# Performance work log

Measured on AMD Instinct MI355X. Metric: run time of the kernel, lower is better.

Reference implementation:

```python
import jax, jax.numpy as jnp
import numpy as np

N_HEADS = 16
D_HEAD = 64
TOKENS_PER_FRAME = 128
ROPE_THETA = 10000.0


def setup_inputs() -> dict:
    key = jax.random.key(0)
    ks = jax.random.split(key, 4)
    B, L, D = 2, 2048, 1024
    x = jax.random.normal(ks[0], (B, L, D), dtype=jnp.float32)
    W_qkv = jax.random.normal(ks[1], (3 * D, D), dtype=jnp.float32) * (1.0 / np.sqrt(D))
    b_qkv = jnp.zeros((3 * D,), dtype=jnp.float32)
    W_out = jax.random.normal(ks[2], (D, D), dtype=jnp.float32) * (1.0 / np.sqrt(D))
    b_out = jnp.zeros((D,), dtype=jnp.float32)
    q_gamma = jnp.ones((D_HEAD,), dtype=jnp.float32)
    k_gamma = jnp.ones((D_HEAD,), dtype=jnp.float32)
    return {"x": x, "W_qkv": W_qkv, "b_qkv": b_qkv, "W_out": W_out,
            "b_out": b_out, "q_gamma": q_gamma, "k_gamma": k_gamma}


def _rms_norm(t, gamma, eps=1e-6):
    # RMSNorm over the head dim (QKNorm)
    var = jnp.mean(jnp.square(t), axis=-1, keepdims=True)
    return t * jax.lax.rsqrt(var + eps) * gamma


def _rope(t, pos):
    # t: [B,H,L,dh], pos: [L] absolute positions (with kv-cache offset applied)
    dh = t.shape[-1]
    half = dh // 2
    inv_freq = 1.0 / (ROPE_THETA ** (jnp.arange(half, dtype=jnp.float32) / half))
    angles = pos[:, None].astype(jnp.float32) * inv_freq[None, :]  # [L, half]
    cos = jnp.cos(angles)[None, None]  # [1,1,L,half]
    sin = jnp.sin(angles)[None, None]
    t1, t2 = t[..., :half], t[..., half:]
    return jnp.concatenate([t1 * cos - t2 * sin, t2 * cos + t1 * sin], axis=-1)


def _block_causal_mask(L, tokens_per_frame, n_cached=0):
    total = n_cached + L
    n_frames = total // tokens_per_frame
    fq = (jnp.arange(L) + n_cached) // tokens_per_frame          # [L] query frames
    fk = jnp.arange(total) // tokens_per_frame                    # [total] key frames
    allow = fk[None, :] <= fq[:, None]
    allow &= ~((fq[:, None] == n_frames - 1) & (fk[None, :] == 0))
    return allow  # [L, total] bool


def reference(x, W_qkv, b_qkv, W_out, b_out, q_gamma, k_gamma):
    B, L, D = x.shape
    H, dh = N_HEADS, D_HEAD
    qkv = x @ W_qkv.T + b_qkv                                    # [B,L,3D]
    qkv = qkv.reshape(B, L, 3, H, dh).transpose(2, 0, 3, 1, 4)   # [3,B,H,L,dh]
    q, k, v = qkv[0], qkv[1], qkv[2]
    q = _rms_norm(q, q_gamma)
    k = _rms_norm(k, k_gamma)
    offset = 0  # no kv_cache (prefill)
    pos = jnp.arange(L) + offset
    q = _rope(q, pos)
    k = _rope(k, jnp.arange(offset + L))
    scale = 1.0 / np.sqrt(dh)
    scores = jnp.einsum('bhqd,bhkd->bhqk', q, k) * scale
    mask = _block_causal_mask(L, TOKENS_PER_FRAME, offset)        # [L, L+offset]
    scores = jnp.where(mask[None, None], scores, jnp.finfo(scores.dtype).min)
    probs = jax.nn.softmax(scores, axis=-1)
    attn = jnp.einsum('bhqk,bhkd->bhqd', probs, v)                # [B,H,L,dh]
    attn = attn.transpose(0, 2, 1, 3).reshape(B, L, D)
    return attn @ W_out.T + b_out
```

## Files before the change

kernel.cpp:

```cpp
#include <hip/hip_runtime.h>
#include <hip/hip_bf16.h>

typedef __bf16 bf16x8 __attribute__((ext_vector_type(8)));
typedef __bf16 bf16x4 __attribute__((ext_vector_type(4)));
typedef float  f32x4  __attribute__((ext_vector_type(4)));

#define GLOBAL_AS __attribute__((address_space(1)))
#define LDS_AS    __attribute__((address_space(3)))

__device__ __forceinline__ void glds16(const void* g, void* l) {
  __builtin_amdgcn_global_load_lds((const GLOBAL_AS void*)g, (LDS_AS void*)l, 16, 0, 0);
}

__global__ __launch_bounds__(256) void prep_kernel(
    const float* __restrict__ a, __bf16* __restrict__ da, int na4,
    const float* __restrict__ b, __bf16* __restrict__ db, int nb4,
    const float* __restrict__ c, __bf16* __restrict__ dc, int nc4,
    float2* __restrict__ tab) {
  int i = blockIdx.x * 256 + threadIdx.x;
  const float* s; __bf16* d; int j = i;
  if (i < na4) { s = a; d = da; }
  else if ((j = i - na4) < nb4) { s = b; d = db; }
  else if ((j = i - na4 - nb4) < nc4) { s = c; d = dc; }
  else {
    j = i - na4 - nb4 - nc4;
    if (j < 65536) {
      int l = j >> 5, jj = j & 31;
      float inv = 1.0f / powf(10000.0f, (float)jj * (1.0f / 32.0f));
      float ang = (float)l * inv;
      tab[j] = make_float2(cosf(ang), sinf(ang));
    }
    return;
  }
  float4 f = ((const float4*)s)[j];
  bf16x4 o;
  o[0] = (__bf16)f.x; o[1] = (__bf16)f.y; o[2] = (__bf16)f.z; o[3] = (__bf16)f.w;
  ((bf16x4*)d)[j] = o;
}

template <int EPI>
__global__ __launch_bounds__(256) void gemm_bt(
    const __bf16* __restrict__ A, const __bf16* __restrict__ Bm, int K, int nbn,
    const float* __restrict__ bias,
    __bf16* __restrict__ qo, __bf16* __restrict__ ko, __bf16* __restrict__ vo,
    float* __restrict__ out,
    const float* __restrict__ qg, const float* __restrict__ kg,
    const float2* __restrict__ tab) {
  __shared__ __bf16 As[128 * 32];
  __shared__ __bf16 Bs[128 * 32];
  const int t = threadIdx.x;
  const int nwg = gridDim.x;
  const int id = blockIdx.x;
  const int swz = (id & 7) * (nwg >> 3) + (id >> 3);
  const int bn = swz % nbn, bm = swz / nbn;
  const int lane = t & 63, w = t >> 6;
  const int wr = w >> 1, wc = w & 1;
  const int lr = lane & 15, lg = lane >> 4;
  const size_t rowA0 = (size_t)bm * 128, rowB0 = (size_t)bn * 128;

  f32x4 acc[4][4] = {};

  for (int k0 = 0; k0 < K; k0 += 32) {
    __syncthreads();
#pragma unroll
    for (int i = 0; i < 2; ++i) {
      int c = t + i * 256;
      int rr = c >> 2, c8 = (c & 3) * 8;
      glds16(A + (rowA0 + rr) * K + k0 + c8, As + c * 8);
      glds16(Bm + (rowB0 + rr) * K + k0 + c8, Bs + c * 8);
    }
    __syncthreads();
    bf16x8 af[4], bfr[4];
#pragma unroll
    for (int i = 0; i < 4; ++i) {
      af[i]  = *(const bf16x8*)&As[(wr * 64 + i * 16 + lr) * 32 + lg * 8];
      bfr[i] = *(const bf16x8*)&Bs[(wc * 64 + i * 16 + lr) * 32 + lg * 8];
    }
#pragma unroll
    for (int mi = 0; mi < 4; ++mi)
#pragma unroll
      for (int ni = 0; ni < 4; ++ni)
        acc[mi][ni] = __builtin_amdgcn_mfma_f32_16x16x32_bf16(af[mi], bfr[ni], acc[mi][ni], 0, 0, 0);
  }

  if constexpr (EPI == 0) {
    const int sect = bn >> 3;
    const int h = (bn * 2 + wc) & 15;
    float bbv[4];
#pragma unroll
    for (int ni = 0; ni < 4; ++ni) bbv[ni] = bias[bn * 128 + wc * 64 + ni * 16 + lr];
    if (sect < 2) {
      __bf16* dst = sect ? ko : qo;
      const float* g = sect ? kg : qg;
      float gam[4];
#pragma unroll
      for (int ni = 0; ni < 4; ++ni) gam[ni] = g[ni * 16 + lr];
#pragma unroll
      for (int mi = 0; mi < 4; ++mi) {
#pragma unroll
        for (int r = 0; r < 4; ++r) {
          int m = bm * 128 + wr * 64 + mi * 16 + lg * 4 + r;
          int b_ = m >> 11, l = m & 2047;
          float v0 = acc[mi][0][r] + bbv[0];
          float v1 = acc[mi][1][r] + bbv[1];
          float v2 = acc[mi][2][r] + bbv[2];
          float v3 = acc[mi][3][r] + bbv[3];
          float ss = v0 * v0 + v1 * v1 + v2 * v2 + v3 * v3;
          ss += __shfl_xor(ss, 1);
          ss += __shfl_xor(ss, 2);
          ss += __shfl_xor(ss, 4);
          ss += __shfl_xor(ss, 8);
          float rinv = rsqrtf(ss * (1.0f / 64.0f) + 1e-6f);
          v0 *= rinv * gam[0]; v1 *= rinv * gam[1];
          v2 *= rinv * gam[2]; v3 *= rinv * gam[3];
          float2 cs0 = tab[l * 32 + lr];
          float2 cs1 = tab[l * 32 + 16 + lr];
          float o0 = v0 * cs0.x - v2 * cs0.y;
          float o2 = v2 * cs0.x + v0 * cs0.y;
          float o1 = v1 * cs1.x - v3 * cs1.y;
          float o3 = v3 * cs1.x + v1 * cs1.y;
          size_t base = ((size_t)(b_ * 16 + h) * 2048 + l) * 64;
          dst[base + lr]      = (__bf16)o0;
          dst[base + 16 + lr] = (__bf16)o1;
          dst[base + 32 + lr] = (__bf16)o2;
          dst[base + 48 + lr] = (__bf16)o3;
        }
      }
    } else {
#pragma unroll
      for (int mi = 0; mi < 4; ++mi) {
#pragma unroll
        for (int ni = 0; ni < 4; ++ni) {
          int d = ni * 16 + lr;
#pragma unroll
          for (int r = 0; r < 4; ++r) {
            int m = bm * 128 + wr * 64 + mi * 16 + lg * 4 + r;
            int b_ = m >> 11, l = m & 2047;
            vo[((size_t)((b_ * 16 + h) * 64 + d)) * 2048 + l] = (__bf16)(acc[mi][ni][r] + bbv[ni]);
          }
        }
      }
    }
  } else {
#pragma unroll
    for (int mi = 0; mi < 4; ++mi) {
      int m0 = bm * 128 + wr * 64 + mi * 16 + lg * 4;
#pragma unroll
      for (int ni = 0; ni < 4; ++ni) {
        int n = bn * 128 + wc * 64 + ni * 16 + lr;
        float bb = bias[n];
#pragma unroll
        for (int r = 0; r < 4; ++r)
          out[(size_t)(m0 + r) * 1024 + n] = acc[mi][ni][r] + bb;
      }
    }
  }
}

__global__ __launch_bounds__(256) void attn_kernel(
    const __bf16* __restrict__ qb, const __bf16* __restrict__ kb,
    const __bf16* __restrict__ vT, __bf16* __restrict__ ob) {
  __shared__ char smem[49152];
  char* Qs = smem;
  char* Ps = smem;

  const int id = blockIdx.x;
  const int rank = (id < 256) ? id : 767 - id;
  const int fq = rank >> 5;
  const int bh = rank & 31;
  const int t = threadIdx.x;
  const int lane = t & 63;
  const int w = t >> 6;
  const int lr = lane & 15, lg = lane >> 4;
  const size_t hoff = (size_t)bh * (2048 * 64);

  const int fkStart = (fq == 15) ? 2 : 0;
  const int fkEnd = (fq + 1) * 2;

#pragma unroll
  for (int i = 0; i < 4; ++i) {
    int c = t + i * 256;
    int row = c >> 3, sl = c & 7;
    int sp = sl ^ (row & 7);
    glds16(qb + hoff + (size_t)(fq * 128 + row) * 64 + sp * 8, Qs + c * 16);
  }
  {
    char* Kd = smem + 16384;
    char* Vd = smem + 32768;
#pragma unroll
    for (int i = 0; i < 2; ++i) {
      int c = t + i * 256;
      int row = c >> 3, sl = c & 7;
      int sp = sl ^ (row & 7);
      glds16(kb + hoff + (size_t)(fkStart * 64 + row) * 64 + sp * 8, Kd + c * 16);
      glds16(vT + hoff + (size_t)row * 2048 + fkStart * 64 + sp * 8, Vd + c * 16);
    }
  }
  bf16x8 kr[2], vr[2];
  if (fkStart + 1 < fkEnd) {
#pragma unroll
    for (int i = 0; i < 2; ++i) {
      int c = t + i * 256;
      int row = c >> 3, sl = c & 7;
      int sp = sl ^ (row & 7);
      kr[i] = *(const bf16x8*)(kb + hoff + (size_t)((fkStart + 1) * 64 + row) * 64 + sp * 8);
      vr[i] = *(const bf16x8*)(vT + hoff + (size_t)row * 2048 + (fkStart + 1) * 64 + sp * 8);
    }
  }
  __syncthreads();

  bf16x8 aq[2][2];
#pragma unroll
  for (int kk = 0; kk < 2; ++kk)
#pragma unroll
    for (int mf = 0; mf < 2; ++mf) {
      int row = w * 32 + mf * 16 + lr;
      aq[kk][mf] = *(const bf16x8*)(Qs + row * 128 + (((kk * 4 + lg) ^ (row & 7)) << 4));
    }
  __syncthreads();

  f32x4 acc[2][4] = {};
  float m_run[2] = {-INFINITY, -INFINITY};
  float l_run[2] = {0.0f, 0.0f};

  int cur = 0;
  for (int fk = fkStart; fk < fkEnd; ++fk) {
    char* Kc = smem + 16384 + cur * 8192;
    char* Vc = smem + 32768 + cur * 8192;
    if (fk + 1 < fkEnd) {
      char* Kd = smem + 16384 + (cur ^ 1) * 8192;
      char* Vd = smem + 32768 + (cur ^ 1) * 8192;
#pragma unroll
      for (int i = 0; i < 2; ++i) {
        int c = t + i * 256;
        *(bf16x8*)(Kd + c * 16) = kr[i];
        *(bf16x8*)(Vd + c * 16) = vr[i];
      }
    }
    if (fk + 2 < fkEnd) {
#pragma unroll
      for (int i = 0; i < 2; ++i) {
        int c = t + i * 256;
        int row = c >> 3, sl = c & 7;
        int sp = sl ^ (row & 7);
        kr[i] = *(const bf16x8*)(kb + hoff + (size_t)((fk + 2) * 64 + row) * 64 + sp * 8);
        vr[i] = *(const bf16x8*)(vT + hoff + (size_t)row * 2048 + (fk + 2) * 64 + sp * 8);
      }
    }

    f32x4 st[2][4] = {};
    __builtin_amdgcn_s_setprio(1);
#pragma unroll
    for (int kk = 0; kk < 2; ++kk) {
#pragma unroll
      for (int nf = 0; nf < 4; ++nf) {
        int rk = nf * 16 + lr;
        bf16x8 bk = *(const bf16x8*)(Kc + rk * 128 + (((kk * 4 + lg) ^ (rk & 7)) << 4));
        st[0][nf] = __builtin_amdgcn_mfma_f32_16x16x32_bf16(bk, aq[kk][0], st[0][nf], 0, 0, 0);
        st[1][nf] = __builtin_amdgcn_mfma_f32_16x16x32_bf16(bk, aq[kk][1], st[1][nf], 0, 0, 0);
      }
    }
    __builtin_amdgcn_s_setprio(0);

#pragma unroll
    for (int mf = 0; mf < 2; ++mf) {
      float mx = st[mf][0][0];
#pragma unroll
      for (int nf = 0; nf < 4; ++nf)
#pragma unroll
        for (int r = 0; r < 4; ++r) mx = fmaxf(mx, st[mf][nf][r]);
      mx *= 0.125f;
      mx = fmaxf(mx, __shfl_xor(mx, 16));
      mx = fmaxf(mx, __shfl_xor(mx, 32));
      float mnew = m_run[mf], cr = 1.0f;
      if (__any(mx > m_run[mf] + 8.0f)) {
        mnew = fmaxf(m_run[mf], mx);
        cr = __expf(m_run[mf] - mnew);
#pragma unroll
        for (int df = 0; df < 4; ++df) acc[mf][df] *= cr;
      }
      float lsum = 0.0f;
#pragma unroll
      for (int nf = 0; nf < 4; ++nf)
#pragma unroll
        for (int r = 0; r < 4; ++r) {
          float p = __expf(st[mf][nf][r] * 0.125f - mnew);
          st[mf][nf][r] = p;
          lsum += p;
        }
      lsum += __shfl_xor(lsum, 16);
      lsum += __shfl_xor(lsum, 32);
      l_run[mf] = l_run[mf] * cr + lsum;
      m_run[mf] = mnew;

#pragma unroll
      for (int nf = 0; nf < 4; ++nf) {
        int row = w * 32 + mf * 16 + lr;
        bf16x4 pw;
#pragma unroll
        for (int r = 0; r < 4; ++r) pw[r] = (__bf16)st[mf][nf][r];
        int slot = nf * 2 + (lg >> 1);
        *(bf16x4*)(Ps + row * 128 + (((slot ^ (row & 7)) << 4) | ((lg & 1) * 8))) = pw;
      }
    }

    __builtin_amdgcn_s_setprio(1);
#pragma unroll
    for (int kk = 0; kk < 2; ++kk) {
      bf16x8 ap[2];
#pragma unroll
      for (int mf = 0; mf < 2; ++mf) {
        int row = w * 32 + mf * 16 + lr;
        ap[mf] = *(const bf16x8*)(Ps + row * 128 + (((kk * 4 + lg) ^ (row & 7)) << 4));
      }
#pragma unroll
      for (int df = 0; df < 4; ++df) {
        int rv = df * 16 + lr;
        bf16x8 av = *(const bf16x8*)(Vc + rv * 128 + (((kk * 4 + lg) ^ (rv & 7)) << 4));
        acc[0][df] = __builtin_amdgcn_mfma_f32_16x16x32_bf16(av, ap[0], acc[0][df], 0, 0, 0);
        acc[1][df] = __builtin_amdgcn_mfma_f32_16x16x32_bf16(av, ap[1], acc[1][df], 0, 0, 0);
      }
    }
    __builtin_amdgcn_s_setprio(0);

    __syncthreads();
    cur ^= 1;
  }

  const int b = bh >> 4, h = bh & 15;
#pragma unroll
  for (int mf = 0; mf < 2; ++mf) {
    float rl = 1.0f / l_run[mf];
    int l = fq * 128 + w * 32 + mf * 16 + lr;
#pragma unroll
    for (int df = 0; df < 4; ++df) {
      bf16x4 ov;
#pragma unroll
      for (int r = 0; r < 4; ++r) ov[r] = (__bf16)(acc[mf][df][r] * rl);
      int d0 = df * 16 + lg * 4;
      *(bf16x4*)(ob + ((size_t)(b * 2048 + l)) * 1024 + h * 64 + d0) = ov;
    }
  }
}

extern "C" void kernel_launch(void* const* d_in, const int* in_sizes, int n_in,
                              void* d_out, int out_size, void* d_ws, size_t ws_size,
                              hipStream_t stream) {
  (void)in_sizes; (void)n_in; (void)out_size; (void)ws_size;
  const float* x    = (const float*)d_in[0];
  const float* Wqkv = (const float*)d_in[1];
  const float* bqkv = (const float*)d_in[2];
  const float* Wout = (const float*)d_in[3];
  const float* bout = (const float*)d_in[4];
  const float* qg   = (const float*)d_in[5];
  const float* kg   = (const float*)d_in[6];

  char* ws = (char*)d_ws;
  __bf16* xb   = (__bf16*)(ws);
  __bf16* wqb  = (__bf16*)(ws + 8388608);
  __bf16* wob  = (__bf16*)(ws + 14680064);
  __bf16* qbuf = (__bf16*)(ws + 16777216);
  __bf16* kbuf = (__bf16*)(ws + 25165824);
  __bf16* vbuf = (__bf16*)(ws + 33554432);
  __bf16* aob  = (__bf16*)(ws + 41943040);
  float2* rtab = (float2*)(ws + 50331648);

  prep_kernel<<<8448, 256, 0, stream>>>(x, xb, 1048576, Wqkv, wqb, 786432,
                                        Wout, wob, 262144, rtab);
  gemm_bt<0><<<768, 256, 0, stream>>>(xb, wqb, 1024, 24, bqkv, qbuf, kbuf, vbuf, nullptr,
                                      qg, kg, rtab);
  attn_kernel<<<512, 256, 0, stream>>>(qbuf, kbuf, vbuf, aob);
  gemm_bt<1><<<256, 256, 0, stream>>>(aob, wob, 1024, 8, bout, nullptr, nullptr, nullptr,
                                      (float*)d_out, nullptr, nullptr, nullptr);
}
```

Before: 203.7 us.

## Split attention into single-wave blocks loading K/V directly from global memory

```diff
diff --git a/kernel.cpp b/kernel.cpp
--- a/kernel.cpp
+++ b/kernel.cpp
@@ -95,24 +95,37 @@
       float gam[4];
 #pragma unroll
       for (int ni = 0; ni < 4; ++ni) gam[ni] = g[ni * 16 + lr];
+      float ss[4][4];
+#pragma unroll
+      for (int mi = 0; mi < 4; ++mi)
+#pragma unroll
+        for (int r = 0; r < 4; ++r) {
+          float s = 0.0f;
+#pragma unroll
+          for (int ni = 0; ni < 4; ++ni) {
+            acc[mi][ni][r] += bbv[ni];
+            s += acc[mi][ni][r] * acc[mi][ni][r];
+          }
+          ss[mi][r] = s;
+        }
+#pragma unroll
+      for (int step = 1; step <= 8; step <<= 1)
+#pragma unroll
+        for (int mi = 0; mi < 4; ++mi)
+#pragma unroll
+          for (int r = 0; r < 4; ++r)
+            ss[mi][r] += __shfl_xor(ss[mi][r], step);
 #pragma unroll
       for (int mi = 0; mi < 4; ++mi) {
 #pragma unroll
         for (int r = 0; r < 4; ++r) {
           int m = bm * 128 + wr * 64 + mi * 16 + lg * 4 + r;
           int b_ = m >> 11, l = m & 2047;
-          float v0 = acc[mi][0][r] + bbv[0];
-          float v1 = acc[mi][1][r] + bbv[1];
-          float v2 = acc[mi][2][r] + bbv[2];
-          float v3 = acc[mi][3][r] + bbv[3];
-          float ss = v0 * v0 + v1 * v1 + v2 * v2 + v3 * v3;
-          ss += __shfl_xor(ss, 1);
-          ss += __shfl_xor(ss, 2);
-          ss += __shfl_xor(ss, 4);
-          ss += __shfl_xor(ss, 8);
-          float rinv = rsqrtf(ss * (1.0f / 64.0f) + 1e-6f);
-          v0 *= rinv * gam[0]; v1 *= rinv * gam[1];
-          v2 *= rinv * gam[2]; v3 *= rinv * gam[3];
+          float rinv = rsqrtf(ss[mi][r] * (1.0f / 64.0f) + 1e-6f);
+          float v0 = acc[mi][0][r] * rinv * gam[0];
+          float v1 = acc[mi][1][r] * rinv * gam[1];
+          float v2 = acc[mi][2][r] * rinv * gam[2];
+          float v3 = acc[mi][3][r] * rinv * gam[3];
           float2 cs0 = tab[l * 32 + lr];
           float2 cs1 = tab[l * 32 + 16 + lr];
           float o0 = v0 * cs0.x - v2 * cs0.y;
@@ -157,110 +170,62 @@
   }
 }
 
-__global__ __launch_bounds__(256) void attn_kernel(
+__global__ __launch_bounds__(64, 3) void attn_kernel(
     const __bf16* __restrict__ qb, const __bf16* __restrict__ kb,
     const __bf16* __restrict__ vT, __bf16* __restrict__ ob) {
-  __shared__ char smem[49152];
-  char* Qs = smem;
-  char* Ps = smem;
+  __shared__ char Ps[4096];
 
   const int id = blockIdx.x;
-  const int rank = (id < 256) ? id : 767 - id;
-  const int fq = rank >> 5;
-  const int bh = rank & 31;
-  const int t = threadIdx.x;
-  const int lane = t & 63;
-  const int w = t >> 6;
+  const int rank = (id < 1024) ? id : 3071 - id;
+  const int fq = rank >> 7;
+  const int bh = (rank >> 2) & 31;
+  const int qq = rank & 3;
+  const int lane = threadIdx.x;
   const int lr = lane & 15, lg = lane >> 4;
   const size_t hoff = (size_t)bh * (2048 * 64);
-
-  const int fkStart = (fq == 15) ? 2 : 0;
-  const int fkEnd = (fq + 1) * 2;
-
-#pragma unroll
-  for (int i = 0; i < 4; ++i) {
-    int c = t + i * 256;
-    int row = c >> 3, sl = c & 7;
-    int sp = sl ^ (row & 7);
-    glds16(qb + hoff + (size_t)(fq * 128 + row) * 64 + sp * 8, Qs + c * 16);
-  }
-  {
-    char* Kd = smem + 16384;
-    char* Vd = smem + 32768;
-#pragma unroll
-    for (int i = 0; i < 2; ++i) {
-      int c = t + i * 256;
-      int row = c >> 3, sl = c & 7;
-      int sp = sl ^ (row & 7);
-      glds16(kb + hoff + (size_t)(fkStart * 64 + row) * 64 + sp * 8, Kd + c * 16);
-      glds16(vT + hoff + (size_t)row * 2048 + fkStart * 64 + sp * 8, Vd + c * 16);
-    }
-  }
-  bf16x8 kr[2], vr[2];
-  if (fkStart + 1 < fkEnd) {
-#pragma unroll
-    for (int i = 0; i < 2; ++i) {
-      int c = t + i * 256;
-      int row = c >> 3, sl = c & 7;
-      int sp = sl ^ (row & 7);
-      kr[i] = *(const bf16x8*)(kb + hoff + (size_t)((fkStart + 1) * 64 + row) * 64 + sp * 8);
-      vr[i] = *(const bf16x8*)(vT + hoff + (size_t)row * 2048 + (fkStart + 1) * 64 + sp * 8);
-    }
-  }
-  __syncthreads();
+  const int q0 = fq * 128 + qq * 32;
 
   bf16x8 aq[2][2];
 #pragma unroll
   for (int kk = 0; kk < 2; ++kk)
 #pragma unroll
-    for (int mf = 0; mf < 2; ++mf) {
-      int row = w * 32 + mf * 16 + lr;
-      aq[kk][mf] = *(const bf16x8*)(Qs + row * 128 + (((kk * 4 + lg) ^ (row & 7)) << 4));
-    }
-  __syncthreads();
+    for (int mf = 0; mf < 2; ++mf)
+      aq[kk][mf] = *(const bf16x8*)(qb + hoff + (size_t)(q0 + mf * 16 + lr) * 64 + kk * 32 + lg * 8);
 
   f32x4 acc[2][4] = {};
   float m_run[2] = {-INFINITY, -INFINITY};
   float l_run[2] = {0.0f, 0.0f};
 
-  int cur = 0;
-  for (int fk = fkStart; fk < fkEnd; ++fk) {
-    char* Kc = smem + 16384 + cur * 8192;
-    char* Vc = smem + 32768 + cur * 8192;
-    if (fk + 1 < fkEnd) {
-      char* Kd = smem + 16384 + (cur ^ 1) * 8192;
-      char* Vd = smem + 32768 + (cur ^ 1) * 8192;
-#pragma unroll
-      for (int i = 0; i < 2; ++i) {
-        int c = t + i * 256;
-        *(bf16x8*)(Kd + c * 16) = kr[i];
-        *(bf16x8*)(Vd + c * 16) = vr[i];
-      }
-    }
-    if (fk + 2 < fkEnd) {
-#pragma unroll
-      for (int i = 0; i < 2; ++i) {
-        int c = t + i * 256;
-        int row = c >> 3, sl = c & 7;
-        int sp = sl ^ (row & 7);
-        kr[i] = *(const bf16x8*)(kb + hoff + (size_t)((fk + 2) * 64 + row) * 64 + sp * 8);
-        vr[i] = *(const bf16x8*)(vT + hoff + (size_t)row * 2048 + (fk + 2) * 64 + sp * 8);
-      }
-    }
+  const int fkS = (fq == 15) ? 2 : 0;
+  const int fkE = (fq + 1) * 2;
+
+  for (int fk = fkS; fk < fkE; ++fk) {
+    const __bf16* kbase = kb + hoff + (size_t)(fk * 64) * 64;
+    bf16x8 kf[2][4];
+#pragma unroll
+    for (int nf = 0; nf < 4; ++nf)
+#pragma unroll
+      for (int kk = 0; kk < 2; ++kk)
+        kf[kk][nf] = *(const bf16x8*)(kbase + (nf * 16 + lr) * 64 + kk * 32 + lg * 8);
 
     f32x4 st[2][4] = {};
     __builtin_amdgcn_s_setprio(1);
 #pragma unroll
-    for (int kk = 0; kk < 2; ++kk) {
+    for (int kk = 0; kk < 2; ++kk)
 #pragma unroll
       for (int nf = 0; nf < 4; ++nf) {
-        int rk = nf * 16 + lr;
-        bf16x8 bk = *(const bf16x8*)(Kc + rk * 128 + (((kk * 4 + lg) ^ (rk & 7)) << 4));
-        st[0][nf] = __builtin_amdgcn_mfma_f32_16x16x32_bf16(bk, aq[kk][0], st[0][nf], 0, 0, 0);
-        st[1][nf] = __builtin_amdgcn_mfma_f32_16x16x32_bf16(bk, aq[kk][1], st[1][nf], 0, 0, 0);
-      }
-    }
+        st[0][nf] = __builtin_amdgcn_mfma_f32_16x16x32_bf16(kf[kk][nf], aq[kk][0], st[0][nf], 0, 0, 0);
+        st[1][nf] = __builtin_amdgcn_mfma_f32_16x16x32_bf16(kf[kk][nf], aq[kk][1], st[1][nf], 0, 0, 0);
+      }
     __builtin_amdgcn_s_setprio(0);
+
+    const __bf16* vbase = vT + hoff + fk * 64;
+    bf16x8 vf[2][4];
+#pragma unroll
+    for (int df = 0; df < 4; ++df)
+#pragma unroll
+      for (int kk = 0; kk < 2; ++kk)
+        vf[kk][df] = *(const bf16x8*)(vbase + (size_t)(df * 16 + lr) * 2048 + kk * 32 + lg * 8);
 
 #pragma unroll
     for (int mf = 0; mf < 2; ++mf) {
@@ -284,7 +249,7 @@
       for (int nf = 0; nf < 4; ++nf)
 #pragma unroll
         for (int r = 0; r < 4; ++r) {
-          float p = __expf(st[mf][nf][r] * 0.125f - mnew);
+          float p = __expf(fmaf(st[mf][nf][r], 0.125f, -mnew));
           st[mf][nf][r] = p;
           lsum += p;
         }
@@ -295,12 +260,12 @@
 
 #pragma unroll
       for (int nf = 0; nf < 4; ++nf) {
-        int row = w * 32 + mf * 16 + lr;
+        int row = mf * 16 + lr;
         bf16x4 pw;
 #pragma unroll
         for (int r = 0; r < 4; ++r) pw[r] = (__bf16)st[mf][nf][r];
         int slot = nf * 2 + (lg >> 1);
-        *(bf16x4*)(Ps + row * 128 + (((slot ^ (row & 7)) << 4) | ((lg & 1) * 8))) = pw;
+        *(bf16x4*)(Ps + row * 128 + (((slot ^ (lr & 7)) << 4) | ((lg & 1) * 8))) = pw;
       }
     }
 
@@ -310,28 +275,23 @@
       bf16x8 ap[2];
 #pragma unroll
       for (int mf = 0; mf < 2; ++mf) {
-        int row = w * 32 + mf * 16 + lr;
-        ap[mf] = *(const bf16x8*)(Ps + row * 128 + (((kk * 4 + lg) ^ (row & 7)) << 4));
+        int row = mf * 16 + lr;
+        ap[mf] = *(const bf16x8*)(Ps + row * 128 + (((kk * 4 + lg) ^ (lr & 7)) << 4));
       }
 #pragma unroll
       for (int df = 0; df < 4; ++df) {
-        int rv = df * 16 + lr;
-        bf16x8 av = *(const bf16x8*)(Vc + rv * 128 + (((kk * 4 + lg) ^ (rv & 7)) << 4));
-        acc[0][df] = __builtin_amdgcn_mfma_f32_16x16x32_bf16(av, ap[0], acc[0][df], 0, 0, 0);
-        acc[1][df] = __builtin_amdgcn_mfma_f32_16x16x32_bf16(av, ap[1], acc[1][df], 0, 0, 0);
+        acc[0][df] = __builtin_amdgcn_mfma_f32_16x16x32_bf16(vf[kk][df], ap[0], acc[0][df], 0, 0, 0);
+        acc[1][df] = __builtin_amdgcn_mfma_f32_16x16x32_bf16(vf[kk][df], ap[1], acc[1][df], 0, 0, 0);
       }
     }
     __builtin_amdgcn_s_setprio(0);
-
-    __syncthreads();
-    cur ^= 1;
   }
 
   const int b = bh >> 4, h = bh & 15;
 #pragma unroll
   for (int mf = 0; mf < 2; ++mf) {
     float rl = 1.0f / l_run[mf];
-    int l = fq * 128 + w * 32 + mf * 16 + lr;
+    int l = q0 + mf * 16 + lr;
 #pragma unroll
     for (int df = 0; df < 4; ++df) {
       bf16x4 ov;
@@ -369,7 +329,7 @@
                                         Wout, wob, 262144, rtab);
   gemm_bt<0><<<768, 256, 0, stream>>>(xb, wqb, 1024, 24, bqkv, qbuf, kbuf, vbuf, nullptr,
                                       qg, kg, rtab);
-  attn_kernel<<<512, 256, 0, stream>>>(qbuf, kbuf, vbuf, aob);
+  attn_kernel<<<2048, 64, 0, stream>>>(qbuf, kbuf, vbuf, aob);
   gemm_bt<1><<<256, 256, 0, stream>>>(aob, wob, 1024, 8, bout, nullptr, nullptr, nullptr,
                                       (float*)d_out, nullptr, nullptr, nullptr);
 }
```

After: 236.0 us. +15.9%, slower.
